# Kernel tuning notes

Hardware: AMD Instinct MI355X
Metric: run time of the kernel (lower is better)

Reference implementation:

```python
import jax, jax.numpy as jnp
import numpy as np

CAT_CARDS = [10, 20, 15, 8, 30, 12, 5, 25, 6, 40, 18, 9]   # categorical_card entries with card > 1 (first 20 entries)
NUM = 32          # num_numerical
NBIN = 8          # categorical_card[:-2] entries with card == 1
NLIKE = 2         # last two categorical_card entries, both card 1
NMASK = NUM + len(CAT_CARDS) + NBIN + NLIKE   # 32 + 22 = 54 mask heads
LAT, HID, B = 128, 1024, 16384
TAU = 1.0
EPS = 1e-20


def setup_inputs() -> dict:
    key = jax.random.key(0)
    ks = jax.random.split(key, 7)
    w = lambda k, sh: (jax.random.normal(k, sh, jnp.float32) * 0.02)
    return {
        "z": jax.random.normal(ks[0], (B, LAT), jnp.float32),
        "W1": w(ks[1], (LAT, HID)), "b1": jnp.zeros((HID,), jnp.float32),
        "W_num": w(ks[2], (HID, NUM)), "b_num": jnp.zeros((NUM,), jnp.float32),
        "W_cat": w(ks[3], (HID, sum(CAT_CARDS))), "b_cat": jnp.zeros((sum(CAT_CARDS),), jnp.float32),
        "W_bin": w(ks[4], (HID, NBIN)), "b_bin": jnp.zeros((NBIN,), jnp.float32),
        "W_like": w(ks[5], (HID, NLIKE)), "b_like": jnp.zeros((NLIKE,), jnp.float32),
        "W_mask": w(ks[6], (HID, NMASK)), "b_mask": jnp.zeros((NMASK,), jnp.float32),
    }


def _gumbel_sigmoid(logits, key, tau=TAU):
    # matches torch: noise~U(0,1); g = -log(-log(noise+eps)+eps); sigmoid((logits+g)/tau); hard=False
    u = jax.random.uniform(key, logits.shape, logits.dtype)
    g = -jnp.log(-jnp.log(u + EPS) + EPS)
    return jax.nn.sigmoid((logits + g) / tau)


def reference(z, W1, b1, W_num, b_num, W_cat, b_cat, W_bin, b_bin, W_like, b_like, W_mask, b_mask):
    nk = jax.random.split(jax.random.key(1), 3)
    h = jax.nn.relu(z @ W1 + b1)                       # [B, HID]
    num_out = h @ W_num + b_num                        # [B, NUM]

    cat_logits = h @ W_cat + b_cat                     # [B, sum(cards)] fused GEMM, then split per head
    splits = np.cumsum(CAT_CARDS)[:-1].tolist()
    cat_out = tuple(jnp.split(cat_logits, splits, axis=1))

    # use_gumbel=True, hard=False: binary / likewise / mask heads get gumbel-sigmoid
    bin_out = _gumbel_sigmoid(h @ W_bin + b_bin, nk[0])      # [B, NBIN]
    like_out = _gumbel_sigmoid(h @ W_like + b_like, nk[1])   # [B, NLIKE]
    mask_out = _gumbel_sigmoid(h @ W_mask + b_mask, nk[2])   # [B, NMASK]

    bins = tuple(bin_out[:, i:i + 1] for i in range(NBIN))
    likes = tuple(like_out[:, i:i + 1] for i in range(NLIKE))
    masks = tuple(mask_out[:, i:i + 1] for i in range(NMASK))
    return (num_out,) + cat_out + bins + likes + masks
```

## Files before the change

### kernel.cpp

```cpp
#include <hip/hip_runtime.h>
#include <stdint.h>

#define B_ROWS 16384
#define LATD   128
#define HIDD   1024

typedef __bf16 bf16x8 __attribute__((ext_vector_type(8)));
typedef float  f32x4  __attribute__((ext_vector_type(4)));
typedef float  f32x4v __attribute__((ext_vector_type(4)));
typedef unsigned short ushort8v __attribute__((ext_vector_type(8)));
typedef unsigned int   uint2v   __attribute__((ext_vector_type(2)));

template<int N> __device__ __forceinline__ void waitv() {
  asm volatile("s_waitcnt vmcnt(%0)" :: "i"(N) : "memory");
  __builtin_amdgcn_sched_barrier(0);
}
__device__ __forceinline__ void gl16(bf16x8& r, const unsigned short* p) {
  asm volatile("global_load_dwordx4 %0, %1, off" : "=v"(r) : "v"(p));
}
template<int OFF> __device__ __forceinline__ void gl16o(bf16x8& r, const unsigned short* p) {
  asm volatile("global_load_dwordx4 %0, %1, off offset:%2" : "=v"(r) : "v"(p), "i"(OFF));
}
#define LGKM_BARRIER() do {                                        \
    asm volatile("s_waitcnt lgkmcnt(0)" ::: "memory");             \
    __builtin_amdgcn_s_barrier();                                  \
    asm volatile("" ::: "memory");                                 \
  } while (0)

struct TF2 { unsigned int a, b; };

#define TF_R(x0,x1,r) { x0 += x1; x1 = ((x1 << (r)) | (x1 >> (32 - (r)))); x1 ^= x0; }

__host__ __device__ constexpr TF2 threefry2x32(unsigned k0, unsigned k1, unsigned c0, unsigned c1) {
  unsigned ks2 = k0 ^ k1 ^ 0x1BD11BDAu;
  unsigned x0 = c0 + k0, x1 = c1 + k1;
  TF_R(x0,x1,13) TF_R(x0,x1,15) TF_R(x0,x1,26) TF_R(x0,x1,6)
  x0 += k1;  x1 += ks2 + 1u;
  TF_R(x0,x1,17) TF_R(x0,x1,29) TF_R(x0,x1,16) TF_R(x0,x1,24)
  x0 += ks2; x1 += k0 + 2u;
  TF_R(x0,x1,13) TF_R(x0,x1,15) TF_R(x0,x1,26) TF_R(x0,x1,6)
  x0 += k0;  x1 += k1 + 3u;
  TF_R(x0,x1,17) TF_R(x0,x1,29) TF_R(x0,x1,16) TF_R(x0,x1,24)
  x0 += k1;  x1 += ks2 + 4u;
  TF_R(x0,x1,13) TF_R(x0,x1,15) TF_R(x0,x1,26) TF_R(x0,x1,6)
  x0 += ks2; x1 += k0 + 5u;
  return {x0, x1};
}

constexpr TF2 NK0 = threefry2x32(0u, 1u, 0u, 0u);
constexpr TF2 NK1 = threefry2x32(0u, 1u, 0u, 1u);
constexpr TF2 NK2 = threefry2x32(0u, 1u, 0u, 2u);

__device__ __forceinline__ unsigned short f2bf(float f) {
  unsigned u = __float_as_uint(f);
  return (unsigned short)((u + 0x7fffu + ((u >> 16) & 1u)) >> 16);
}

__global__ __launch_bounds__(256) void prep_kernel(
    const float* __restrict__ W1,
    const float* __restrict__ Wnum, const float* __restrict__ Wcat,
    const float* __restrict__ Wbin, const float* __restrict__ Wlike,
    const float* __restrict__ Wmask,
    const float* __restrict__ bnum, const float* __restrict__ bcat,
    const float* __restrict__ bbin, const float* __restrict__ blike,
    const float* __restrict__ bmask,
    unsigned short* __restrict__ W1p,
    unsigned short* __restrict__ Wallp,
    float* __restrict__ ball) {
  __shared__ __align__(16) unsigned short lds[8704];
  const int b = blockIdx.x, t = threadIdx.x;

  if (b < 16) {
    const int n0 = b * 64;
    #pragma unroll
    for (int i = 0; i < 8; ++i) {
      int linear = i * 256 + t;
      int k = linear >> 4, nq = linear & 15;
      f32x4 v = *(const f32x4*)(W1 + (size_t)k * HIDD + n0 + nq * 4);
      #pragma unroll
      for (int e = 0; e < 4; ++e) lds[(nq * 4 + e) * 136 + k] = f2bf(v[e]);
    }
    __syncthreads();
    #pragma unroll
    for (int i = 0; i < 4; ++i) {
      int linear = i * 256 + t;
      int f_loc = linear >> 6, l = linear & 63;
      int l15 = l & 15, l4 = l >> 4;
      int n_loc = (f_loc >> 2) * 16 + l15;
      int k = (f_loc & 3) * 32 + l4 * 8;
      ushort8v p = *(const ushort8v*)(lds + n_loc * 136 + k);
      *(ushort8v*)(W1p + ((size_t)(b * 16 + f_loc) * 64 + l) * 8) = p;
    }
  } else if (b < 96) {
    const int q  = b - 16;
    const int nt = q >> 2, ktb = q & 3;
    const int n0 = nt * 16, k0 = ktb * 256;
    const int n = n0 + (t & 15);
    #pragma unroll
    for (int i = 0; i < 16; ++i) {
      int kk_loc = i * 16 + (t >> 4);
      int kk = k0 + kk_loc;
      float v = 0.f;
      if (n < 32)       v = Wnum [(size_t)kk * 32  + n];
      else if (n < 230) v = Wcat [(size_t)kk * 198 + (n - 32)];
      else if (n < 238) v = Wbin [(size_t)kk * 8   + (n - 230)];
      else if (n < 240) v = Wlike[(size_t)kk * 2   + (n - 238)];
      else if (n < 294) v = Wmask[(size_t)kk * 54  + (n - 240)];
      lds[(t & 15) * 264 + kk_loc] = f2bf(v);
    }
    __syncthreads();
    #pragma unroll
    for (int i = 0; i < 2; ++i) {
      int linear = i * 256 + t;
      int kt_loc = linear >> 6, l = linear & 63;
      int l15 = l & 15, l4 = l >> 4;
      int koff = kt_loc * 32 + l4 * 8;
      ushort8v p = *(const ushort8v*)(lds + l15 * 264 + koff);
      int g = nt * 32 + ktb * 8 + kt_loc;
      *(ushort8v*)(Wallp + ((size_t)g * 64 + l) * 8) = p;
    }
  } else {
    for (int n = t; n < 320; n += 256) {
      float v = 0.f;
      if (n < 32)       v = bnum [n];
      else if (n < 230) v = bcat [n - 32];
      else if (n < 238) v = bbin [n - 230];
      else if (n < 240) v = blike[n - 238];
      else if (n < 294) v = bmask[n - 240];
      ball[n] = v;
    }
  }
}

template<int G>
__device__ __forceinline__ void run_phases(
    const int w, const int lane, const int l15, const int l4, const int nt0,
    const unsigned short* __restrict__ W1p, const unsigned short* __restrict__ Wallp,
    const float* __restrict__ b1,
    unsigned char* smem, f32x4 (&acc)[4][3]) {

  unsigned short* zs = (unsigned short*)smem;
  unsigned char* hbase  = smem + 17408;
  unsigned char* mytile = hbase + w * 16384;

  f32x4 hb1[8];
  #pragma unroll
  for (int ct = 0; ct < 8; ++ct)
    hb1[ct] = *(const f32x4*)(b1 + w * 128 + ct * 16 + l4 * 4);

  bf16x8 za[4][4];
  #pragma unroll
  for (int rt = 0; rt < 4; ++rt)
    #pragma unroll
    for (int ks = 0; ks < 4; ++ks)
      za[rt][ks] = *(const bf16x8*)(zs + (rt * 16 + l15) * 136 + ks * 32 + l4 * 8);

  bf16x8 wq1[2][4];
  const unsigned short* w1b = W1p + (size_t)w * 16384 + lane * 8;
  #pragma unroll
  for (int ct = 0; ct < 2; ++ct) {
    const unsigned short* p = w1b + ct * 2048;
    gl16o<0>(wq1[ct][0], p); gl16o<1024>(wq1[ct][1], p);
    gl16o<2048>(wq1[ct][2], p); gl16o<3072>(wq1[ct][3], p);
  }

  bf16x8 wq2[4][G];
  const unsigned short* w2b = Wallp + lane * 8;

  #pragma unroll
  for (int ct = 0; ct < 8; ++ct) {
    if (ct < 7) waitv<4>();
    else        waitv<G * 4>();
    f32x4 a[4] = {};
    __builtin_amdgcn_s_setprio(1);
    #pragma unroll
    for (int ks = 0; ks < 4; ++ks)
      #pragma unroll
      for (int rt = 0; rt < 4; ++rt)
        a[rt] = __builtin_amdgcn_mfma_f32_16x16x32_bf16(wq1[ct & 1][ks], za[rt][ks], a[rt], 0, 0, 0);
    __builtin_amdgcn_s_setprio(0);
    #pragma unroll
    for (int rt = 0; rt < 4; ++rt) {
      float v0 = fmaxf(a[rt][0] + hb1[ct][0], 0.f);
      float v1 = fmaxf(a[rt][1] + hb1[ct][1], 0.f);
      float v2 = fmaxf(a[rt][2] + hb1[ct][2], 0.f);
      float v3 = fmaxf(a[rt][3] + hb1[ct][3], 0.f);
      uint2v u;
      u[0] = (unsigned)f2bf(v0) | ((unsigned)f2bf(v1) << 16);
      u[1] = (unsigned)f2bf(v2) | ((unsigned)f2bf(v3) << 16);
      const int byte = ((ct >> 1) * 4 + rt) * 1024
                     + ((ct & 1) * 2 + (l4 >> 1)) * 256
                     + l15 * 16 + (l4 & 1) * 8;
      *(uint2v*)(mytile + byte) = u;
    }
    if (ct < 6) {
      const unsigned short* p = w1b + (ct + 2) * 2048;
      gl16o<0>(wq1[ct & 1][0], p); gl16o<1024>(wq1[ct & 1][1], p);
      gl16o<2048>(wq1[ct & 1][2], p); gl16o<3072>(wq1[ct & 1][3], p);
    } else if (ct == 6) {
      #pragma unroll
      for (int g = 0; g < 4; ++g)
        #pragma unroll
        for (int cc = 0; cc < G; ++cc)
          gl16(wq2[g][cc], w2b + (size_t)((nt0 + cc) * 32 + g) * 512);
    }
  }

  LGKM_BARRIER();

  #pragma unroll
  for (int rt = 0; rt < 4; ++rt)
    #pragma unroll
    for (int ct = 0; ct < 3; ++ct)
      acc[rt][ct] = (f32x4){0.f, 0.f, 0.f, 0.f};

  #pragma unroll
  for (int g = 0; g < 32; ++g) {
    if (g < 29)       waitv<G * 3>();
    else if (g == 29) waitv<G * 2>();
    else if (g == 30) waitv<G>();
    else              waitv<0>();
    const unsigned char* hc = hbase + (g >> 2) * 16384 + (g & 3) * 4096 + lane * 16;
    __builtin_amdgcn_s_setprio(1);
    #pragma unroll
    for (int rt = 0; rt < 4; ++rt) {
      bf16x8 ha = *(const bf16x8*)(hc + rt * 1024);
      #pragma unroll
      for (int ct = 0; ct < G; ++ct)
        acc[rt][ct] = __builtin_amdgcn_mfma_f32_16x16x32_bf16(ha, wq2[g & 3][ct], acc[rt][ct], 0, 0, 0);
    }
    __builtin_amdgcn_s_setprio(0);
    if (g + 4 < 32) {
      #pragma unroll
      for (int cc = 0; cc < G; ++cc)
        gl16(wq2[g & 3][cc], w2b + (size_t)((nt0 + cc) * 32 + (g + 4)) * 512);
    }
  }
}

__global__ __launch_bounds__(512, 2) void decoder_kernel(
    const float* __restrict__ z, const float* __restrict__ b1,
    const unsigned short* __restrict__ W1p, const unsigned short* __restrict__ Wallp,
    const float* __restrict__ ball, float* __restrict__ out) {
  __shared__ __align__(16) unsigned char smem[148480];
  unsigned short* zs = (unsigned short*)smem;
  float* outs = (float*)smem;

  const int tid  = threadIdx.x;
  const int lane = tid & 63;
  const int w    = tid >> 6;
  const int l15  = lane & 15;
  const int l4   = lane >> 4;
  const int r0   = blockIdx.x * 64;

  #pragma unroll
  for (int it = 0; it < 2; ++it) {
    int ch  = tid + it * 512;
    int row = ch >> 4;
    int k0  = (ch & 15) * 8;
    const float* src = z + (size_t)(r0 + row) * LATD + k0;
    f32x4v f0 = __builtin_nontemporal_load((const f32x4v*)src);
    f32x4v f1 = __builtin_nontemporal_load((const f32x4v*)(src + 4));
    ushort8v p;
    p[0] = f2bf(f0[0]); p[1] = f2bf(f0[1]); p[2] = f2bf(f0[2]); p[3] = f2bf(f0[3]);
    p[4] = f2bf(f1[0]); p[5] = f2bf(f1[1]); p[6] = f2bf(f1[2]); p[7] = f2bf(f1[3]);
    *(ushort8v*)(zs + row * 136 + k0) = p;
  }
  __syncthreads();

  const int cb  = (w < 4) ? w * 48 : 192 + (w - 4) * 32;
  const int nt0 = (w < 4) ? w * 3  : 12 + (w - 4) * 2;
  const int myG = (w < 4) ? 3 : 2;

  f32x4 acc[4][3];
  if (w < 4) run_phases<3>(w, lane, l15, l4, nt0, W1p, Wallp, b1, smem, acc);
  else       run_phases<2>(w, lane, l15, l4, nt0, W1p, Wallp, b1, smem, acc);

  __syncthreads();

  #pragma unroll
  for (int ct = 0; ct < 3; ++ct) {
    if (ct < myG) {
      float b2 = ball[cb + ct * 16 + l15];
      #pragma unroll
      for (int rt = 0; rt < 4; ++rt)
        #pragma unroll
        for (int j = 0; j < 4; ++j)
          outs[(rt * 16 + l4 * 4 + j) * 321 + cb + ct * 16 + l15] = acc[rt][ct][j] + b2;
    }
  }
  __syncthreads();

  {
    constexpr int cards[13] = {32,10,20,15,8,30,12,5,25,6,40,18,9};
    constexpr int cbase[13] = {0,32,42,62,77,85,115,127,132,157,163,203,221};
    #pragma unroll
    for (int blk = 0; blk < 13; ++blk) {
      const int card = cards[blk];
      const int cbs  = cbase[blk];
      float* gout = out + (size_t)B_ROWS * cbs + (size_t)r0 * card;
      for (int v = tid; v < card * 16; v += 512) {
        int gg = v * 4;
        f32x4v vbuf;
        #pragma unroll
        for (int e = 0; e < 4; ++e) {
          int ge = gg + e;
          int brow = ge / card;
          int j = ge - brow * card;
          vbuf[e] = outs[brow * 321 + cbs + j];
        }
        __builtin_nontemporal_store(vbuf, (f32x4v*)(gout + gg));
      }
    }
  }

  {
    int c = 230 + (tid >> 3);
    unsigned ka, kb; int Nh, head;
    if (c < 238)      { ka = NK0.a; kb = NK0.b; Nh = 8;  head = c - 230; }
    else if (c < 240) { ka = NK1.a; kb = NK1.b; Nh = 2;  head = c - 238; }
    else              { ka = NK2.a; kb = NK2.b; Nh = 54; head = c - 240; }
    #pragma unroll
    for (int q = 0; q < 2; ++q) {
      int rq = (tid & 7) * 4 + q * 32;
      f32x4v vbuf;
      #pragma unroll
      for (int e = 0; e < 4; ++e) {
        int rl = rq + e;
        float x = outs[rl * 321 + c];
        unsigned j = (unsigned)((r0 + rl) * Nh + head);
        TF2 t = threefry2x32(ka, kb, 0u, j);
        unsigned bits = t.a ^ t.b;
        float u  = __uint_as_float((bits >> 9) | 0x3f800000u) - 1.0f;
        float gn = -__logf(-__logf(u + 1e-20f) + 1e-20f);
        vbuf[e] = 1.0f / (1.0f + __expf(-(x + gn)));
      }
      __builtin_nontemporal_store(vbuf, (f32x4v*)(out + (size_t)B_ROWS * c + r0 + rq));
    }
  }
}

extern "C" void kernel_launch(void* const* d_in, const int* in_sizes, int n_in,
                              void* d_out, int out_size, void* d_ws, size_t ws_size,
                              hipStream_t stream) {
  const float* z     = (const float*)d_in[0];
  const float* W1    = (const float*)d_in[1];
  const float* b1    = (const float*)d_in[2];
  const float* Wnum  = (const float*)d_in[3];
  const float* bnum  = (const float*)d_in[4];
  const float* Wcat  = (const float*)d_in[5];
  const float* bcat  = (const float*)d_in[6];
  const float* Wbin  = (const float*)d_in[7];
  const float* bbin  = (const float*)d_in[8];
  const float* Wlike = (const float*)d_in[9];
  const float* blike = (const float*)d_in[10];
  const float* Wmask = (const float*)d_in[11];
  const float* bmask = (const float*)d_in[12];

  unsigned short* W1p   = (unsigned short*)d_ws;
  unsigned short* Wallp = W1p + 131072;
  float*          ball  = (float*)(Wallp + 327680);

  prep_kernel<<<97, 256, 0, stream>>>(
      W1, Wnum, Wcat, Wbin, Wlike, Wmask, bnum, bcat, bbin, blike, bmask,
      W1p, Wallp, ball);

  decoder_kernel<<<B_ROWS / 64, 512, 0, stream>>>(
      z, b1, W1p, Wallp, ball, (float*)d_out);
}
```

Baseline: 30.24 us.

## Prefetch W1 before z staging, split epilogue work, drop setprio hints

Issues the first W1 fragment loads at kernel start, so they overlap the z load, conversion and LDS staging, and replaces that __syncthreads with an lgkmcnt-only barrier. It removes the s_setprio bracketing around the MFMA loops and relaxes the sched_barrier mask in the second GEMM's waits so the compiler can move more instructions across them. The epilogue now splits threads: half write the categorical and numeric columns while the other half compute the Gumbel-sigmoid heads, instead of every thread doing both in sequence. In exchange, the W1 fragments stay live in registers for longer, and the per-thread Gumbel work doubles on the threads that do it.

```diff
diff --git a/kernel.cpp b/kernel.cpp
--- a/kernel.cpp
+++ b/kernel.cpp
@@ -14,6 +14,10 @@
 template<int N> __device__ __forceinline__ void waitv() {
   asm volatile("s_waitcnt vmcnt(%0)" :: "i"(N) : "memory");
   __builtin_amdgcn_sched_barrier(0);
+}
+template<int N> __device__ __forceinline__ void waitv2() {
+  asm volatile("s_waitcnt vmcnt(%0)" :: "i"(N) : "memory");
+  __builtin_amdgcn_sched_barrier(0x2 | 0x4 | 0x100 | 0x200);
 }
 __device__ __forceinline__ void gl16(bf16x8& r, const unsigned short* p) {
   asm volatile("global_load_dwordx4 %0, %1, off" : "=v"(r) : "v"(p));
@@ -137,7 +141,7 @@
     const int w, const int lane, const int l15, const int l4, const int nt0,
     const unsigned short* __restrict__ W1p, const unsigned short* __restrict__ Wallp,
     const float* __restrict__ b1,
-    unsigned char* smem, f32x4 (&acc)[4][3]) {
+    unsigned char* smem, bf16x8 (&wq1)[2][4], f32x4 (&acc)[4][3]) {
 
   unsigned short* zs = (unsigned short*)smem;
   unsigned char* hbase  = smem + 17408;
@@ -155,15 +159,7 @@
     for (int ks = 0; ks < 4; ++ks)
       za[rt][ks] = *(const bf16x8*)(zs + (rt * 16 + l15) * 136 + ks * 32 + l4 * 8);
 
-  bf16x8 wq1[2][4];
   const unsigned short* w1b = W1p + (size_t)w * 16384 + lane * 8;
-  #pragma unroll
-  for (int ct = 0; ct < 2; ++ct) {
-    const unsigned short* p = w1b + ct * 2048;
-    gl16o<0>(wq1[ct][0], p); gl16o<1024>(wq1[ct][1], p);
-    gl16o<2048>(wq1[ct][2], p); gl16o<3072>(wq1[ct][3], p);
-  }
-
   bf16x8 wq2[4][G];
   const unsigned short* w2b = Wallp + lane * 8;
 
@@ -172,13 +168,11 @@
     if (ct < 7) waitv<4>();
     else        waitv<G * 4>();
     f32x4 a[4] = {};
-    __builtin_amdgcn_s_setprio(1);
     #pragma unroll
     for (int ks = 0; ks < 4; ++ks)
       #pragma unroll
       for (int rt = 0; rt < 4; ++rt)
         a[rt] = __builtin_amdgcn_mfma_f32_16x16x32_bf16(wq1[ct & 1][ks], za[rt][ks], a[rt], 0, 0, 0);
-    __builtin_amdgcn_s_setprio(0);
     #pragma unroll
     for (int rt = 0; rt < 4; ++rt) {
       float v0 = fmaxf(a[rt][0] + hb1[ct][0], 0.f);
@@ -216,12 +210,11 @@
 
   #pragma unroll
   for (int g = 0; g < 32; ++g) {
-    if (g < 29)       waitv<G * 3>();
-    else if (g == 29) waitv<G * 2>();
-    else if (g == 30) waitv<G>();
-    else              waitv<0>();
+    if (g < 29)       waitv2<G * 3>();
+    else if (g == 29) waitv2<G * 2>();
+    else if (g == 30) waitv2<G>();
+    else              waitv2<0>();
     const unsigned char* hc = hbase + (g >> 2) * 16384 + (g & 3) * 4096 + lane * 16;
-    __builtin_amdgcn_s_setprio(1);
     #pragma unroll
     for (int rt = 0; rt < 4; ++rt) {
       bf16x8 ha = *(const bf16x8*)(hc + rt * 1024);
@@ -229,7 +222,6 @@
       for (int ct = 0; ct < G; ++ct)
         acc[rt][ct] = __builtin_amdgcn_mfma_f32_16x16x32_bf16(ha, wq2[g & 3][ct], acc[rt][ct], 0, 0, 0);
     }
-    __builtin_amdgcn_s_setprio(0);
     if (g + 4 < 32) {
       #pragma unroll
       for (int cc = 0; cc < G; ++cc)
@@ -252,6 +244,17 @@
   const int l15  = lane & 15;
   const int l4   = lane >> 4;
   const int r0   = blockIdx.x * 64;
+
+  bf16x8 wq1[2][4];
+  {
+    const unsigned short* w1b = W1p + (size_t)w * 16384 + lane * 8;
+    #pragma unroll
+    for (int ct = 0; ct < 2; ++ct) {
+      const unsigned short* p = w1b + ct * 2048;
+      gl16o<0>(wq1[ct][0], p); gl16o<1024>(wq1[ct][1], p);
+      gl16o<2048>(wq1[ct][2], p); gl16o<3072>(wq1[ct][3], p);
+    }
+  }
 
   #pragma unroll
   for (int it = 0; it < 2; ++it) {
@@ -266,15 +269,15 @@
     p[4] = f2bf(f1[0]); p[5] = f2bf(f1[1]); p[6] = f2bf(f1[2]); p[7] = f2bf(f1[3]);
     *(ushort8v*)(zs + row * 136 + k0) = p;
   }
-  __syncthreads();
+  LGKM_BARRIER();
 
   const int cb  = (w < 4) ? w * 48 : 192 + (w - 4) * 32;
   const int nt0 = (w < 4) ? w * 3  : 12 + (w - 4) * 2;
   const int myG = (w < 4) ? 3 : 2;
 
   f32x4 acc[4][3];
-  if (w < 4) run_phases<3>(w, lane, l15, l4, nt0, W1p, Wallp, b1, smem, acc);
-  else       run_phases<2>(w, lane, l15, l4, nt0, W1p, Wallp, b1, smem, acc);
+  if (w < 4) run_phases<3>(w, lane, l15, l4, nt0, W1p, Wallp, b1, smem, wq1, acc);
+  else       run_phases<2>(w, lane, l15, l4, nt0, W1p, Wallp, b1, smem, wq1, acc);
 
   __syncthreads();
 
@@ -291,7 +294,7 @@
   }
   __syncthreads();
 
-  {
+  if (tid < 256) {
     constexpr int cards[13] = {32,10,20,15,8,30,12,5,25,6,40,18,9};
     constexpr int cbase[13] = {0,32,42,62,77,85,115,127,132,157,163,203,221};
     #pragma unroll
@@ -299,7 +302,7 @@
       const int card = cards[blk];
       const int cbs  = cbase[blk];
       float* gout = out + (size_t)B_ROWS * cbs + (size_t)r0 * card;
-      for (int v = tid; v < card * 16; v += 512) {
+      for (int v = tid; v < card * 16; v += 256) {
         int gg = v * 4;
         f32x4v vbuf;
         #pragma unroll
@@ -312,25 +315,24 @@
         __builtin_nontemporal_store(vbuf, (f32x4v*)(gout + gg));
       }
     }
-  }
-
-  {
-    int c = 230 + (tid >> 3);
+  } else {
+    int t = tid - 256;
+    int c = 230 + (t >> 2);
     unsigned ka, kb; int Nh, head;
     if (c < 238)      { ka = NK0.a; kb = NK0.b; Nh = 8;  head = c - 230; }
     else if (c < 240) { ka = NK1.a; kb = NK1.b; Nh = 2;  head = c - 238; }
     else              { ka = NK2.a; kb = NK2.b; Nh = 54; head = c - 240; }
     #pragma unroll
-    for (int q = 0; q < 2; ++q) {
-      int rq = (tid & 7) * 4 + q * 32;
+    for (int q = 0; q < 4; ++q) {
+      int rq = (t & 3) * 16 + q * 4;
       f32x4v vbuf;
       #pragma unroll
       for (int e = 0; e < 4; ++e) {
         int rl = rq + e;
         float x = outs[rl * 321 + c];
         unsigned j = (unsigned)((r0 + rl) * Nh + head);
-        TF2 t = threefry2x32(ka, kb, 0u, j);
-        unsigned bits = t.a ^ t.b;
+        TF2 tt = threefry2x32(ka, kb, 0u, j);
+        unsigned bits = tt.a ^ tt.b;
         float u  = __uint_as_float((bits >> 9) | 0x3f800000u) - 1.0f;
         float gn = -__logf(-__logf(u + 1e-20f) + 1e-20f);
         vbuf[e] = 1.0f / (1.0f + __expf(-(x + gn)));
```

New measurement: 32.43 us. 7.3% more time.
